# Optimization experiments

Measured on AMD Instinct MI355X. Metric: run time of the kernel, lower is better.

Reference implementation:

```python
import jax, jax.numpy as jnp
import numpy as np

D = 64        # state dim (num_output)
H = 256       # MLP hidden width
B = 4096      # batch
NUM_STEPS = 16  # fixed-step Dormand-Prince steps over t in [0,1] per bijector


def _mlp(t, y, W1, b1, W2, b2, W3, b3):
    # time-conditioned MLP: concat scalar t to state, two tanh layers, linear out
    tcol = jnp.full((y.shape[0], 1), t, dtype=y.dtype)
    h = jnp.tanh(jnp.concatenate([y, tcol], axis=1) @ W1 + b1)
    h = jnp.tanh(h @ W2 + b2)
    return h @ W3 + b3


def _dopri5_fixed(f, y0):
    # classic Dormand-Prince (RK45) Butcher tableau, 5th-order solution,
    # fixed step h = 1/NUM_STEPS from t=0 to t=1
    h = jnp.asarray(1.0 / NUM_STEPS, dtype=y0.dtype)

    def step(y, i):
        t = i.astype(y0.dtype) * h
        k1 = f(t, y)
        k2 = f(t + h * (1/5),  y + h * ((1/5) * k1))
        k3 = f(t + h * (3/10), y + h * ((3/40) * k1 + (9/40) * k2))
        k4 = f(t + h * (4/5),  y + h * ((44/45) * k1 - (56/15) * k2 + (32/9) * k3))
        k5 = f(t + h * (8/9),  y + h * ((19372/6561) * k1 - (25360/2187) * k2
                                        + (64448/6561) * k3 - (212/729) * k4))
        k6 = f(t + h,          y + h * ((9017/3168) * k1 - (355/33) * k2
                                        + (46732/5247) * k3 + (49/176) * k4
                                        - (5103/18656) * k5))
        y_next = y + h * ((35/384) * k1 + (500/1113) * k3 + (125/192) * k4
                          - (2187/6784) * k5 + (11/84) * k6)
        return y_next, None

    y_final, _ = jax.lax.scan(step, y0, jnp.arange(NUM_STEPS))
    return y_final


def setup_inputs() -> dict:
    key = jax.random.key(0)
    ks = jax.random.split(key, 7)
    s_in = 1.0 / np.sqrt(D + 1)
    s_h = 1.0 / np.sqrt(H)
    inp = {"x": jax.random.normal(ks[0], (B, D), dtype=jnp.float32)}
    for i, base in enumerate([1, 4]):
        inp[f"p{i}_W1"] = jax.random.normal(ks[base], (D + 1, H), dtype=jnp.float32) * s_in
        inp[f"p{i}_b1"] = jnp.zeros((H,), dtype=jnp.float32)
        inp[f"p{i}_W2"] = jax.random.normal(ks[base + 1], (H, H), dtype=jnp.float32) * s_h
        inp[f"p{i}_b2"] = jnp.zeros((H,), dtype=jnp.float32)
        inp[f"p{i}_W3"] = jax.random.normal(ks[base + 2], (H, D), dtype=jnp.float32) * s_h
        inp[f"p{i}_b3"] = jnp.zeros((D,), dtype=jnp.float32)
    return inp


def reference(x, p0_W1, p0_b1, p0_W2, p0_b2, p0_W3, p0_b3,
              p1_W1, p1_b1, p1_W2, p1_b2, p1_W3, p1_b3):
    # Chain(list(reversed(bijectors))).forward applies bijector 0 first, then 1.
    # FFJORD bijector forward = integrate dz/dt = mlp(t, z) from t=0 to t=1.
    y = x
    params = [(p0_W1, p0_b1, p0_W2, p0_b2, p0_W3, p0_b3),
              (p1_W1, p1_b1, p1_W2, p1_b2, p1_W3, p1_b3)]
    for (W1, b1, W2, b2, W3, b3) in params:
        f = lambda t, z: _mlp(t, z, W1, b1, W2, b2, W3, b3)
        y = _dopri5_fixed(f, y)
    return y
```

## Files before the change

### kernel.cpp

```cpp
#include <hip/hip_runtime.h>

typedef __attribute__((ext_vector_type(8))) short short8;
typedef __attribute__((ext_vector_type(4))) float f32x4;

#define NSTEPS 16

__device__ __forceinline__ unsigned short bf16rne(float f) {
  unsigned int u = __float_as_uint(f);
  u += 0x7FFFu + ((u >> 16) & 1u);
  return (unsigned short)(u >> 16);
}

__device__ __forceinline__ unsigned int pk2(float a, float b) {
  unsigned int r;
  asm("v_cvt_pk_bf16_f32 %0, %1, %2" : "=v"(r) : "v"(a), "v"(b));
  return r;
}

__device__ __forceinline__ float tanh_fast(float x) {
  float e = __builtin_amdgcn_exp2f(x * 2.8853900817779268f);
  return __builtin_fmaf(-2.0f, __builtin_amdgcn_rcpf(e + 1.0f), 1.0f);
}

__global__ void ffjord_setup(const float* __restrict__ W1a, const float* __restrict__ W2a,
                             const float* __restrict__ W3a, const float* __restrict__ W1b,
                             const float* __restrict__ W2b, const float* __restrict__ W3b,
                             unsigned short* __restrict__ ws) {
  int gid = blockIdx.x * blockDim.x + threadIdx.x;
  int bij = gid / 12288;
  int r = gid - bij * 12288;
  const float* W1 = bij ? W1b : W1a;
  const float* W2 = bij ? W2b : W2a;
  const float* W3 = bij ? W3b : W3a;
  unsigned short* o = ws + bij * 98304;
  const float* src;
  int kstride;
  if (r < 2048) {
    int lane = r & 63, nt = (r >> 6) & 15, ks = r >> 10;
    int k0 = ks * 32 + (lane >> 4) * 8, n = nt * 16 + (lane & 15);
    src = W1 + k0 * 256 + n; kstride = 256; o += r * 8;
  } else if (r < 10240) {
    int rr = r - 2048;
    int lane = rr & 63, nt = (rr >> 6) & 15, ks = rr >> 10;
    int k0 = ks * 32 + (lane >> 4) * 8, n = nt * 16 + (lane & 15);
    src = W2 + k0 * 256 + n; kstride = 256; o += 16384 + rr * 8;
  } else {
    int rr = r - 10240;
    int lane = rr & 63, nt = (rr >> 6) & 3, ks = rr >> 8;
    int k0 = ks * 32 + (lane >> 4) * 8, n = nt * 16 + (lane & 15);
    src = W3 + k0 * 64 + n; kstride = 64; o += 81920 + rr * 8;
  }
  #pragma unroll
  for (int j = 0; j < 8; j++) o[j] = bf16rne(src[j * kstride]);
}

__global__ __launch_bounds__(512, 2) void ffjord_main(
    const float* __restrict__ x, float* __restrict__ out,
    const unsigned short* __restrict__ ws,
    const float* __restrict__ W1a, const float* __restrict__ b1a,
    const float* __restrict__ b2a, const float* __restrict__ b3a,
    const float* __restrict__ W1b, const float* __restrict__ b1b,
    const float* __restrict__ b2b, const float* __restrict__ b3b) {
  __shared__ __align__(16) unsigned short zA[1088];
  __shared__ __align__(16) unsigned short h1A[4096];
  __shared__ __align__(16) unsigned short h2A[4096];

  const int tid = threadIdx.x;
  const int wave = tid >> 6;
  const int lane = tid & 63;
  const int cl = lane & 15;
  const int qd = lane >> 4;
  const int row0 = blockIdx.x * 16;

  const int tc0 = wave * 2, tc1 = tc0 + 1;
  const int c0 = wave * 32 + qd * 4;
  const int hoff = wave * 512 + (qd >> 1) * 128 + cl * 8 + 4 * (qd & 1);
  const int zrb = qd * 136 + cl * 8;
  const int w3i = wave & 3;
  const int dl3 = w3i * 16 + qd * 4;
  const int zw = (2 * w3i + (qd >> 1)) * 136 + cl * 8 + 4 * (qd & 1);

  const float hstep = 1.0f / 16.0f;

  f32x4 yc;

  const float A2[5][5] = {
      {1.f / 5.f, 0.f, 0.f, 0.f, 0.f},
      {3.f / 40.f, 9.f / 40.f, 0.f, 0.f, 0.f},
      {44.f / 45.f, -56.f / 15.f, 32.f / 9.f, 0.f, 0.f},
      {19372.f / 6561.f, -25360.f / 2187.f, 64448.f / 6561.f, -212.f / 729.f, 0.f},
      {9017.f / 3168.f, -355.f / 33.f, 46732.f / 5247.f, 49.f / 176.f, -5103.f / 18656.f}};
  const float CT[6] = {0.0f, 0.2f, 0.3f, 0.8f, 8.0f / 9.0f, 1.0f};
  const float BW0 = 35.f / 384.f, BW2 = 500.f / 1113.f, BW3 = 125.f / 192.f,
              BW4 = -2187.f / 6784.f, BW5 = 11.f / 84.f;

  for (int bij = 0; bij < 2; bij++) {
    const unsigned short* wsb = ws + bij * 98304;
    const float* W1 = bij ? W1b : W1a;
    const float* b1 = bij ? b1b : b1a;
    const float* b2 = bij ? b2b : b2a;
    const float* b3 = bij ? b3b : b3a;

    f32x4 b1c0 = *(const f32x4*)(b1 + c0);
    f32x4 b1c1 = *(const f32x4*)(b1 + c0 + 16);
    f32x4 w1t0 = *(const f32x4*)(W1 + 64 * 256 + c0);
    f32x4 w1t1 = *(const f32x4*)(W1 + 64 * 256 + c0 + 16);
    f32x4 b2c0 = *(const f32x4*)(b2 + c0);
    f32x4 b2c1 = *(const f32x4*)(b2 + c0 + 16);
    f32x4 b3c = *(const f32x4*)(b3 + dl3);

    const short8* w1p = (const short8*)wsb;
    const short8* w2p = (const short8*)(wsb + 16384);
    const short8* w3p = (const short8*)(wsb + 81920);
    short8 w1f0[2], w1f1[2];
    #pragma unroll
    for (int ks = 0; ks < 2; ks++) {
      w1f0[ks] = w1p[(ks * 16 + tc0) * 64 + lane];
      w1f1[ks] = w1p[(ks * 16 + tc1) * 64 + lane];
    }
    short8 w2f0[8], w2f1[8];
    #pragma unroll
    for (int ks = 0; ks < 8; ks++) {
      w2f0[ks] = w2p[(ks * 16 + tc0) * 64 + lane];
      w2f1[ks] = w2p[(ks * 16 + tc1) * 64 + lane];
    }
    short8 w3f[8];
    if (wave < 4) {
      #pragma unroll
      for (int ks = 0; ks < 8; ks++)
        w3f[ks] = w3p[(ks * 4 + w3i) * 64 + lane];
    }

    if (bij == 0 && wave < 4) {
      yc = *(const f32x4*)(x + (row0 + cl) * 64 + dl3);
      uint2 pv;
      pv.x = pk2(yc[0], yc[1]);
      pv.y = pk2(yc[2], yc[3]);
      *(uint2*)(zA + zw) = pv;
    }
    __syncthreads();

    for (int step = 0; step < NSTEPS; step++) {
      float stepf = (float)step;
      f32x4 kh[5];
      #pragma unroll
      for (int s = 0; s < 6; s++) {
        float ts = (stepf + CT[s]) * hstep;

        {
          short8 a0 = *(const short8*)(zA + zrb);
          short8 a1 = *(const short8*)(zA + zrb + 544);
          f32x4 acc0, acc1;
          #pragma unroll
          for (int r = 0; r < 4; r++) {
            acc0[r] = __builtin_fmaf(ts, w1t0[r], b1c0[r]);
            acc1[r] = __builtin_fmaf(ts, w1t1[r], b1c1[r]);
          }
          acc0 = __builtin_amdgcn_mfma_f32_16x16x32_bf16(w1f0[0], a0, acc0, 0, 0, 0);
          acc1 = __builtin_amdgcn_mfma_f32_16x16x32_bf16(w1f1[0], a0, acc1, 0, 0, 0);
          acc0 = __builtin_amdgcn_mfma_f32_16x16x32_bf16(w1f0[1], a1, acc0, 0, 0, 0);
          acc1 = __builtin_amdgcn_mfma_f32_16x16x32_bf16(w1f1[1], a1, acc1, 0, 0, 0);
          uint2 pv0, pv1;
          pv0.x = pk2(tanh_fast(acc0[0]), tanh_fast(acc0[1]));
          pv0.y = pk2(tanh_fast(acc0[2]), tanh_fast(acc0[3]));
          pv1.x = pk2(tanh_fast(acc1[0]), tanh_fast(acc1[1]));
          pv1.y = pk2(tanh_fast(acc1[2]), tanh_fast(acc1[3]));
          *(uint2*)(h1A + hoff) = pv0;
          *(uint2*)(h1A + hoff + 256) = pv1;
        }
        __syncthreads();

        {
          f32x4 aA0 = b2c0, aA1 = b2c1;
          f32x4 aB0; aB0[0] = 0.f; aB0[1] = 0.f; aB0[2] = 0.f; aB0[3] = 0.f;
          f32x4 aB1 = aB0;
          #pragma unroll
          for (int ks = 0; ks < 4; ks++) {
            short8 hb = ((const short8*)h1A)[ks * 64 + lane];
            aA0 = __builtin_amdgcn_mfma_f32_16x16x32_bf16(w2f0[ks], hb, aA0, 0, 0, 0);
            aA1 = __builtin_amdgcn_mfma_f32_16x16x32_bf16(w2f1[ks], hb, aA1, 0, 0, 0);
          }
          #pragma unroll
          for (int ks = 4; ks < 8; ks++) {
            short8 hb = ((const short8*)h1A)[ks * 64 + lane];
            aB0 = __builtin_amdgcn_mfma_f32_16x16x32_bf16(w2f0[ks], hb, aB0, 0, 0, 0);
            aB1 = __builtin_amdgcn_mfma_f32_16x16x32_bf16(w2f1[ks], hb, aB1, 0, 0, 0);
          }
          uint2 pv0, pv1;
          pv0.x = pk2(tanh_fast(aA0[0] + aB0[0]), tanh_fast(aA0[1] + aB0[1]));
          pv0.y = pk2(tanh_fast(aA0[2] + aB0[2]), tanh_fast(aA0[3] + aB0[3]));
          pv1.x = pk2(tanh_fast(aA1[0] + aB1[0]), tanh_fast(aA1[1] + aB1[1]));
          pv1.y = pk2(tanh_fast(aA1[2] + aB1[2]), tanh_fast(aA1[3] + aB1[3]));
          *(uint2*)(h2A + hoff) = pv0;
          *(uint2*)(h2A + hoff + 256) = pv1;
        }
        __syncthreads();

        if (wave < 4) {
          f32x4 accP = b3c;
          f32x4 accQ; accQ[0] = 0.f; accQ[1] = 0.f; accQ[2] = 0.f; accQ[3] = 0.f;
          #pragma unroll
          for (int ks = 0; ks < 8; ks += 2) {
            short8 hb0 = ((const short8*)h2A)[ks * 64 + lane];
            short8 hb1 = ((const short8*)h2A)[(ks + 1) * 64 + lane];
            accP = __builtin_amdgcn_mfma_f32_16x16x32_bf16(w3f[ks], hb0, accP, 0, 0, 0);
            accQ = __builtin_amdgcn_mfma_f32_16x16x32_bf16(w3f[ks + 1], hb1, accQ, 0, 0, 0);
          }
          f32x4 kc;
          #pragma unroll
          for (int r = 0; r < 4; r++) kc[r] = accP[r] + accQ[r];

          f32x4 z;
          if (s < 5) {
            kh[s] = kc;
            #pragma unroll
            for (int r = 0; r < 4; r++)
              z[r] = __builtin_fmaf(hstep * A2[s][s], kc[r], yc[r]);
            #pragma unroll
            for (int j = 0; j < 4; j++)
              if (j < s) {
                float a = hstep * A2[s][j];
                #pragma unroll
                for (int r = 0; r < 4; r++) z[r] = __builtin_fmaf(a, kh[j][r], z[r]);
              }
          } else {
            #pragma unroll
            for (int r = 0; r < 4; r++) {
              float d = BW0 * kh[0][r] + BW2 * kh[2][r] + BW3 * kh[3][r] +
                        BW4 * kh[4][r] + BW5 * kc[r];
              yc[r] += hstep * d;
              z[r] = yc[r];
            }
          }
          uint2 pv;
          pv.x = pk2(z[0], z[1]);
          pv.y = pk2(z[2], z[3]);
          *(uint2*)(zA + zw) = pv;
        }
        __syncthreads();
      }
    }
  }

  if (wave < 4)
    *(f32x4*)(out + (row0 + cl) * 64 + dl3) = yc;
}

extern "C" void kernel_launch(void* const* d_in, const int* in_sizes, int n_in,
                              void* d_out, int out_size, void* d_ws, size_t ws_size,
                              hipStream_t stream) {
  (void)in_sizes; (void)n_in; (void)out_size; (void)ws_size;
  const float* x   = (const float*)d_in[0];
  const float* W1a = (const float*)d_in[1];
  const float* b1a = (const float*)d_in[2];
  const float* W2a = (const float*)d_in[3];
  const float* b2a = (const float*)d_in[4];
  const float* W3a = (const float*)d_in[5];
  const float* b3a = (const float*)d_in[6];
  const float* W1b = (const float*)d_in[7];
  const float* b1b = (const float*)d_in[8];
  const float* W2b = (const float*)d_in[9];
  const float* b2b = (const float*)d_in[10];
  const float* W3b = (const float*)d_in[11];
  const float* b3b = (const float*)d_in[12];
  unsigned short* ws = (unsigned short*)d_ws;
  float* out = (float*)d_out;

  hipLaunchKernelGGL(ffjord_setup, dim3(96), dim3(256), 0, stream,
                     W1a, W2a, W3a, W1b, W2b, W3b, ws);
  hipLaunchKernelGGL(ffjord_main, dim3(256), dim3(512), 0, stream,
                     x, out, ws, W1a, b1a, b2a, b3a, W1b, b1b, b2b, b3b);
}
```

Baseline: 298.9 us.

## Fold W3·W1 into a fused matrix to drop a GEMM and a sync per stage

Rewrites the RK stages to carry the first-layer pre-activation u = y·W1 directly. Precomputing M = W3·W1[:64] and b3·W1 lets each stage go straight from h2 to the next h1 input through one 256x256 GEMM, removing the separate z-GEMM, the z staging in shared memory and one barrier per stage. The state y is still advanced with the W3 output, now computed alongside and skipped where its Butcher weight is zero, with W3 fragments cached in LDS. The cost is a heavier per-stage GEMM, more register pressure, a large LDS allocation that may reduce occupancy, and a changed bf16 rounding path.

```diff
diff --git a/kernel.cpp b/kernel.cpp
--- a/kernel.cpp
+++ b/kernel.cpp
@@ -54,6 +54,47 @@
   for (int j = 0; j < 8; j++) o[j] = bf16rne(src[j * kstride]);
 }
 
+__global__ void ffjord_setup2(const float* __restrict__ W1a, const float* __restrict__ W3a,
+                              const float* __restrict__ b3a, const float* __restrict__ W1b,
+                              const float* __restrict__ W3b, const float* __restrict__ b3b,
+                              unsigned short* __restrict__ ws) {
+  int bid = blockIdx.x;
+  int tid = threadIdx.x;
+  if (bid < 64) {
+    int gid = bid * 4 + (tid >> 6);
+    int bij = gid >> 7;
+    int rem = gid & 127;
+    int ks = rem >> 4;
+    int t = rem & 15;
+    int lane = tid & 63;
+    const float* W1 = bij ? W1b : W1a;
+    const float* W3 = bij ? W3b : W3a;
+    int c = t * 16 + (lane & 15);
+    int kb = ks * 32 + (lane >> 4) * 8;
+    float acc[8];
+    #pragma unroll
+    for (int j = 0; j < 8; j++) acc[j] = 0.f;
+    for (int d = 0; d < 64; d++) {
+      float w1d = W1[d * 256 + c];
+      #pragma unroll
+      for (int j = 0; j < 8; j++)
+        acc[j] = __builtin_fmaf(W3[(kb + j) * 64 + d], w1d, acc[j]);
+    }
+    unsigned short* o = ws + 196608 + bij * 65536 + ((ks * 16 + t) * 64 + lane) * 8;
+    #pragma unroll
+    for (int j = 0; j < 8; j++) o[j] = bf16rne(acc[j]);
+  } else {
+    for (int v = tid; v < 512; v += 256) {
+      int bij = v >> 8, c = v & 255;
+      const float* W1 = bij ? W1b : W1a;
+      const float* b3 = bij ? b3b : b3a;
+      float a = 0.f;
+      for (int d = 0; d < 64; d++) a = __builtin_fmaf(W1[d * 256 + c], b3[d], a);
+      ((float*)(ws + 327680))[v] = a;
+    }
+  }
+}
+
 __global__ __launch_bounds__(512, 2) void ffjord_main(
     const float* __restrict__ x, float* __restrict__ out,
     const unsigned short* __restrict__ ws,
@@ -64,6 +105,7 @@
   __shared__ __align__(16) unsigned short zA[1088];
   __shared__ __align__(16) unsigned short h1A[4096];
   __shared__ __align__(16) unsigned short h2A[4096];
+  __shared__ __align__(16) unsigned short w3s[2][16384];
 
   const int tid = threadIdx.x;
   const int wave = tid >> 6;
@@ -93,6 +135,20 @@
   const float CT[6] = {0.0f, 0.2f, 0.3f, 0.8f, 8.0f / 9.0f, 1.0f};
   const float BW0 = 35.f / 384.f, BW2 = 500.f / 1113.f, BW3 = 125.f / 192.f,
               BW4 = -2187.f / 6784.f, BW5 = 11.f / 84.f;
+  const float HBW[6] = {hstep * BW0, 0.f, hstep * BW2, hstep * BW3,
+                        hstep * BW4, hstep * BW5};
+
+  {
+    const uint4* s0 = (const uint4*)(ws + 81920);
+    const uint4* s1 = (const uint4*)(ws + 98304 + 81920);
+    uint4* d0 = (uint4*)&w3s[0][0];
+    uint4* d1 = (uint4*)&w3s[1][0];
+    #pragma unroll
+    for (int i = 0; i < 4; i++) {
+      d0[tid + i * 512] = s0[tid + i * 512];
+      d1[tid + i * 512] = s1[tid + i * 512];
+    }
+  }
 
   for (int bij = 0; bij < 2; bij++) {
     const unsigned short* wsb = ws + bij * 98304;
@@ -107,32 +163,24 @@
     f32x4 w1t1 = *(const f32x4*)(W1 + 64 * 256 + c0 + 16);
     f32x4 b2c0 = *(const f32x4*)(b2 + c0);
     f32x4 b2c1 = *(const f32x4*)(b2 + c0 + 16);
+    f32x4 cb3c0 = *(const f32x4*)((const float*)(ws + 327680) + bij * 256 + c0);
+    f32x4 cb3c1 = *(const f32x4*)((const float*)(ws + 327680) + bij * 256 + c0 + 16);
     f32x4 b3c = *(const f32x4*)(b3 + dl3);
 
-    const short8* w1p = (const short8*)wsb;
     const short8* w2p = (const short8*)(wsb + 16384);
-    const short8* w3p = (const short8*)(wsb + 81920);
-    short8 w1f0[2], w1f1[2];
-    #pragma unroll
-    for (int ks = 0; ks < 2; ks++) {
-      w1f0[ks] = w1p[(ks * 16 + tc0) * 64 + lane];
-      w1f1[ks] = w1p[(ks * 16 + tc1) * 64 + lane];
-    }
-    short8 w2f0[8], w2f1[8];
+    const short8* mp = (const short8*)(ws + 196608 + bij * 65536);
+    short8 w2f0[8], w2f1[8], mf0[8], mf1[8];
     #pragma unroll
     for (int ks = 0; ks < 8; ks++) {
       w2f0[ks] = w2p[(ks * 16 + tc0) * 64 + lane];
       w2f1[ks] = w2p[(ks * 16 + tc1) * 64 + lane];
-    }
-    short8 w3f[8];
+      mf0[ks] = mp[(ks * 16 + tc0) * 64 + lane];
+      mf1[ks] = mp[(ks * 16 + tc1) * 64 + lane];
+    }
+    const short8* w3c = (const short8*)&w3s[bij][0];
+
     if (wave < 4) {
-      #pragma unroll
-      for (int ks = 0; ks < 8; ks++)
-        w3f[ks] = w3p[(ks * 4 + w3i) * 64 + lane];
-    }
-
-    if (bij == 0 && wave < 4) {
-      yc = *(const f32x4*)(x + (row0 + cl) * 64 + dl3);
+      if (bij == 0) yc = *(const f32x4*)(x + (row0 + cl) * 64 + dl3);
       uint2 pv;
       pv.x = pk2(yc[0], yc[1]);
       pv.y = pk2(yc[2], yc[3]);
@@ -140,40 +188,44 @@
     }
     __syncthreads();
 
+    f32x4 uy0, uy1;
+    {
+      const short8* w1p = (const short8*)wsb;
+      short8 wA0 = w1p[(0 * 16 + tc0) * 64 + lane];
+      short8 wA1 = w1p[(1 * 16 + tc0) * 64 + lane];
+      short8 wB0 = w1p[(0 * 16 + tc1) * 64 + lane];
+      short8 wB1 = w1p[(1 * 16 + tc1) * 64 + lane];
+      short8 a0 = *(const short8*)(zA + zrb);
+      short8 a1 = *(const short8*)(zA + zrb + 544);
+      f32x4 r0, r1;
+      #pragma unroll
+      for (int r = 0; r < 4; r++) { r0[r] = 0.f; r1[r] = 0.f; }
+      r0 = __builtin_amdgcn_mfma_f32_16x16x32_bf16(wA0, a0, r0, 0, 0, 0);
+      r1 = __builtin_amdgcn_mfma_f32_16x16x32_bf16(wB0, a0, r1, 0, 0, 0);
+      r0 = __builtin_amdgcn_mfma_f32_16x16x32_bf16(wA1, a1, r0, 0, 0, 0);
+      r1 = __builtin_amdgcn_mfma_f32_16x16x32_bf16(wB1, a1, r1, 0, 0, 0);
+      uy0 = r0;
+      uy1 = r1;
+      uint2 pv0, pv1;
+      pv0.x = pk2(tanh_fast(r0[0] + b1c0[0]), tanh_fast(r0[1] + b1c0[1]));
+      pv0.y = pk2(tanh_fast(r0[2] + b1c0[2]), tanh_fast(r0[3] + b1c0[3]));
+      pv1.x = pk2(tanh_fast(r1[0] + b1c1[0]), tanh_fast(r1[1] + b1c1[1]));
+      pv1.y = pk2(tanh_fast(r1[2] + b1c1[2]), tanh_fast(r1[3] + b1c1[3]));
+      *(uint2*)(h1A + hoff) = pv0;
+      *(uint2*)(h1A + hoff + 256) = pv1;
+    }
+    __syncthreads();
+
     for (int step = 0; step < NSTEPS; step++) {
       float stepf = (float)step;
-      f32x4 kh[5];
+      f32x4 uh0[5], uh1[5];
       #pragma unroll
       for (int s = 0; s < 6; s++) {
-        float ts = (stepf + CT[s]) * hstep;
-
-        {
-          short8 a0 = *(const short8*)(zA + zrb);
-          short8 a1 = *(const short8*)(zA + zrb + 544);
-          f32x4 acc0, acc1;
-          #pragma unroll
-          for (int r = 0; r < 4; r++) {
-            acc0[r] = __builtin_fmaf(ts, w1t0[r], b1c0[r]);
-            acc1[r] = __builtin_fmaf(ts, w1t1[r], b1c1[r]);
-          }
-          acc0 = __builtin_amdgcn_mfma_f32_16x16x32_bf16(w1f0[0], a0, acc0, 0, 0, 0);
-          acc1 = __builtin_amdgcn_mfma_f32_16x16x32_bf16(w1f1[0], a0, acc1, 0, 0, 0);
-          acc0 = __builtin_amdgcn_mfma_f32_16x16x32_bf16(w1f0[1], a1, acc0, 0, 0, 0);
-          acc1 = __builtin_amdgcn_mfma_f32_16x16x32_bf16(w1f1[1], a1, acc1, 0, 0, 0);
-          uint2 pv0, pv1;
-          pv0.x = pk2(tanh_fast(acc0[0]), tanh_fast(acc0[1]));
-          pv0.y = pk2(tanh_fast(acc0[2]), tanh_fast(acc0[3]));
-          pv1.x = pk2(tanh_fast(acc1[0]), tanh_fast(acc1[1]));
-          pv1.y = pk2(tanh_fast(acc1[2]), tanh_fast(acc1[3]));
-          *(uint2*)(h1A + hoff) = pv0;
-          *(uint2*)(h1A + hoff + 256) = pv1;
-        }
-        __syncthreads();
-
         {
           f32x4 aA0 = b2c0, aA1 = b2c1;
-          f32x4 aB0; aB0[0] = 0.f; aB0[1] = 0.f; aB0[2] = 0.f; aB0[3] = 0.f;
-          f32x4 aB1 = aB0;
+          f32x4 aB0, aB1;
+          #pragma unroll
+          for (int r = 0; r < 4; r++) { aB0[r] = 0.f; aB1[r] = 0.f; }
           #pragma unroll
           for (int ks = 0; ks < 4; ks++) {
             short8 hb = ((const short8*)h1A)[ks * 64 + lane];
@@ -196,46 +248,96 @@
         }
         __syncthreads();
 
-        if (wave < 4) {
-          f32x4 accP = b3c;
-          f32x4 accQ; accQ[0] = 0.f; accQ[1] = 0.f; accQ[2] = 0.f; accQ[3] = 0.f;
-          #pragma unroll
-          for (int ks = 0; ks < 8; ks += 2) {
-            short8 hb0 = ((const short8*)h2A)[ks * 64 + lane];
-            short8 hb1 = ((const short8*)h2A)[(ks + 1) * 64 + lane];
-            accP = __builtin_amdgcn_mfma_f32_16x16x32_bf16(w3f[ks], hb0, accP, 0, 0, 0);
-            accQ = __builtin_amdgcn_mfma_f32_16x16x32_bf16(w3f[ks + 1], hb1, accQ, 0, 0, 0);
-          }
-          f32x4 kc;
-          #pragma unroll
-          for (int r = 0; r < 4; r++) kc[r] = accP[r] + accQ[r];
-
-          f32x4 z;
+        {
+          f32x4 uA0 = cb3c0, uA1 = cb3c1;
+          f32x4 uB0, uB1;
+          #pragma unroll
+          for (int r = 0; r < 4; r++) { uB0[r] = 0.f; uB1[r] = 0.f; }
+          f32x4 accP, accQ;
+          const bool dok = (s != 1);
+          if (dok && wave < 4) {
+            accP = b3c;
+            #pragma unroll
+            for (int r = 0; r < 4; r++) accQ[r] = 0.f;
+          }
+          #pragma unroll
+          for (int ks = 0; ks < 8; ks++) {
+            short8 hb = ((const short8*)h2A)[ks * 64 + lane];
+            if (ks < 4) {
+              uA0 = __builtin_amdgcn_mfma_f32_16x16x32_bf16(mf0[ks], hb, uA0, 0, 0, 0);
+              uA1 = __builtin_amdgcn_mfma_f32_16x16x32_bf16(mf1[ks], hb, uA1, 0, 0, 0);
+            } else {
+              uB0 = __builtin_amdgcn_mfma_f32_16x16x32_bf16(mf0[ks], hb, uB0, 0, 0, 0);
+              uB1 = __builtin_amdgcn_mfma_f32_16x16x32_bf16(mf1[ks], hb, uB1, 0, 0, 0);
+            }
+            if (dok && wave < 4) {
+              short8 wf = w3c[(ks * 4 + w3i) * 64 + lane];
+              if ((ks & 1) == 0)
+                accP = __builtin_amdgcn_mfma_f32_16x16x32_bf16(wf, hb, accP, 0, 0, 0);
+              else
+                accQ = __builtin_amdgcn_mfma_f32_16x16x32_bf16(wf, hb, accQ, 0, 0, 0);
+            }
+          }
+          f32x4 uc0, uc1;
+          #pragma unroll
+          for (int r = 0; r < 4; r++) {
+            uc0[r] = uA0[r] + uB0[r];
+            uc1[r] = uA1[r] + uB1[r];
+          }
+          if (dok && wave < 4) {
+            #pragma unroll
+            for (int r = 0; r < 4; r++)
+              yc[r] = __builtin_fmaf(HBW[s], accP[r] + accQ[r], yc[r]);
+          }
+
+          float tnext = (s < 5) ? (stepf + CT[s + 1]) * hstep
+                                : (stepf + 1.0f) * hstep;
+          f32x4 p0, p1;
           if (s < 5) {
-            kh[s] = kc;
-            #pragma unroll
-            for (int r = 0; r < 4; r++)
-              z[r] = __builtin_fmaf(hstep * A2[s][s], kc[r], yc[r]);
+            uh0[s] = uc0;
+            uh1[s] = uc1;
+            float ad = hstep * A2[s][s];
+            #pragma unroll
+            for (int r = 0; r < 4; r++) {
+              p0[r] = __builtin_fmaf(tnext, w1t0[r], b1c0[r]) + uy0[r];
+              p1[r] = __builtin_fmaf(tnext, w1t1[r], b1c1[r]) + uy1[r];
+              p0[r] = __builtin_fmaf(ad, uc0[r], p0[r]);
+              p1[r] = __builtin_fmaf(ad, uc1[r], p1[r]);
+            }
             #pragma unroll
             for (int j = 0; j < 4; j++)
               if (j < s) {
                 float a = hstep * A2[s][j];
                 #pragma unroll
-                for (int r = 0; r < 4; r++) z[r] = __builtin_fmaf(a, kh[j][r], z[r]);
+                for (int r = 0; r < 4; r++) {
+                  p0[r] = __builtin_fmaf(a, uh0[j][r], p0[r]);
+                  p1[r] = __builtin_fmaf(a, uh1[j][r], p1[r]);
+                }
               }
           } else {
             #pragma unroll
             for (int r = 0; r < 4; r++) {
-              float d = BW0 * kh[0][r] + BW2 * kh[2][r] + BW3 * kh[3][r] +
-                        BW4 * kh[4][r] + BW5 * kc[r];
-              yc[r] += hstep * d;
-              z[r] = yc[r];
+              float d0 = __builtin_fmaf(BW0, uh0[0][r],
+                         __builtin_fmaf(BW2, uh0[2][r],
+                         __builtin_fmaf(BW3, uh0[3][r],
+                         __builtin_fmaf(BW4, uh0[4][r], BW5 * uc0[r]))));
+              float d1 = __builtin_fmaf(BW0, uh1[0][r],
+                         __builtin_fmaf(BW2, uh1[2][r],
+                         __builtin_fmaf(BW3, uh1[3][r],
+                         __builtin_fmaf(BW4, uh1[4][r], BW5 * uc1[r]))));
+              uy0[r] = __builtin_fmaf(hstep, d0, uy0[r]);
+              uy1[r] = __builtin_fmaf(hstep, d1, uy1[r]);
+              p0[r] = __builtin_fmaf(tnext, w1t0[r], b1c0[r]) + uy0[r];
+              p1[r] = __builtin_fmaf(tnext, w1t1[r], b1c1[r]) + uy1[r];
             }
           }
-          uint2 pv;
-          pv.x = pk2(z[0], z[1]);
-          pv.y = pk2(z[2], z[3]);
-          *(uint2*)(zA + zw) = pv;
+          uint2 pv0, pv1;
+          pv0.x = pk2(tanh_fast(p0[0]), tanh_fast(p0[1]));
+          pv0.y = pk2(tanh_fast(p0[2]), tanh_fast(p0[3]));
+          pv1.x = pk2(tanh_fast(p1[0]), tanh_fast(p1[1]));
+          pv1.y = pk2(tanh_fast(p1[2]), tanh_fast(p1[3]));
+          *(uint2*)(h1A + hoff) = pv0;
+          *(uint2*)(h1A + hoff + 256) = pv1;
         }
         __syncthreads();
       }
@@ -268,6 +370,8 @@
 
   hipLaunchKernelGGL(ffjord_setup, dim3(96), dim3(256), 0, stream,
                      W1a, W2a, W3a, W1b, W2b, W3b, ws);
+  hipLaunchKernelGGL(ffjord_setup2, dim3(65), dim3(256), 0, stream,
+                     W1a, W3a, b3a, W1b, W3b, b3b, ws);
   hipLaunchKernelGGL(ffjord_main, dim3(256), dim3(512), 0, stream,
                      x, out, ws, W1a, b1a, b2a, b3a, W1b, b1b, b2b, b3b);
 }
```

After: 624.0 us. 2.09x slower.
